# Kernel optimization log

Hardware: AMD Instinct MI355X
Metric: run time of the kernel (lower is better)

Reference implementation:

```python
import jax, jax.numpy as jnp
import numpy as np

N = 50000          # nodes (spots/cells)
E = 1000000        # edges, avg degree 20
IN_DIM, HID, OUT = 256, 128, 64
R = 2              # num_relations
NEG_SLOPE = 0.2    # PyG RGATConv default


def setup_inputs() -> dict:
    key = jax.random.key(0)
    ks = jax.random.split(key, 12)
    features = jax.random.normal(ks[0], (N, IN_DIM), jnp.float32)
    edge_index = jax.random.randint(ks[1], (2, E), 0, N)
    edge_type = jax.random.randint(ks[2], (E,), 0, R)
    s_in, s_hid, s_out = 1.0 / np.sqrt(IN_DIM), 1.0 / np.sqrt(HID), 1.0 / np.sqrt(OUT)
    # RGATConv layer 1 (heads=1, dim=1): relation weights + shared q,k
    W1 = jax.random.normal(ks[3], (R, IN_DIM, HID), jnp.float32) * s_in
    q1 = jax.random.normal(ks[4], (HID, 1), jnp.float32) * s_hid
    k1 = jax.random.normal(ks[5], (HID, 1), jnp.float32) * s_hid
    # RGATConv layer 2
    W2 = jax.random.normal(ks[6], (R, HID, OUT), jnp.float32) * s_hid
    q2 = jax.random.normal(ks[7], (OUT, 1), jnp.float32) * s_out
    k2 = jax.random.normal(ks[8], (OUT, 1), jnp.float32) * s_out
    # decoder: Linear(OUT->HID) then Linear(HID->IN_DIM), biases default-on
    dec_w1 = jax.random.normal(ks[9], (HID, OUT), jnp.float32) * s_out
    dec_b1 = jnp.zeros((HID,), jnp.float32)
    dec_w2 = jax.random.normal(ks[10], (IN_DIM, HID), jnp.float32) * s_hid
    dec_b2 = jnp.zeros((IN_DIM,), jnp.float32)
    return dict(features=features, edge_index=edge_index, edge_type=edge_type,
                W1=W1, q1=q1, k1=k1, W2=W2, q2=q2, k2=k2,
                dec_w1=dec_w1, dec_b1=dec_b1, dec_w2=dec_w2, dec_b2=dec_b2)


def _segment_softmax(alpha, index, num_segments):
    # softmax over edges grouped by destination node (PyG softmax, +1e-16 denom)
    amax = jax.ops.segment_max(alpha, index, num_segments=num_segments)
    amax = jnp.where(jnp.isfinite(amax), amax, 0.0)  # empty segments -> -inf
    ex = jnp.exp(alpha - amax[index])
    denom = jax.ops.segment_sum(ex, index, num_segments=num_segments)
    return ex / (denom[index] + 1e-16)


def _rgat_layer(x, W, q, k, src, dst, edge_type, num_nodes):
    # per-edge x_e @ W[edge_type[e]] == project all nodes per relation, then gather
    proj = jnp.einsum('ni,rio->rno', x, W)          # (R, N, O)
    out_i = proj[edge_type, dst]                    # (E, O) dest-node projection
    out_j = proj[edge_type, src]                    # (E, O) src-node projection
    alpha = jax.nn.leaky_relu(out_i @ q + out_j @ k, NEG_SLOPE)  # (E, 1)
    alpha = _segment_softmax(alpha, dst, num_nodes)
    out = jax.ops.segment_sum(alpha * out_j, dst, num_segments=num_nodes)  # (N, O)
    return out, alpha


def reference(features, edge_index, edge_type, W1, q1, k1, W2, q2, k2,
              dec_w1, dec_b1, dec_w2, dec_b2):
    src, dst = edge_index[0], edge_index[1]
    n = features.shape[0]
    h1, att1 = _rgat_layer(features, W1, q1, k1, src, dst, edge_type, n)
    h1 = jax.nn.elu(h1)
    h2, att2 = _rgat_layer(h1, W2, q2, k2, src, dst, edge_type, n)
    h2 = jax.nn.elu(h2)
    h3 = (h2 @ dec_w1.T + dec_b1) @ dec_w2.T + dec_b2
    return h2, h3, att1, att2
```

## Files before the change

kernel.cpp:

```cpp
#include <hip/hip_runtime.h>
#include <hip/hip_bf16.h>

static constexpr int N_NODES = 50000;
static constexpr int N_EDGE  = 1000000;
static constexpr int IN_D    = 256;
static constexpr int HID_D   = 128;
static constexpr int OUT_D   = 64;
static constexpr int R_REL   = 2;

typedef __attribute__((ext_vector_type(8))) short short8;
typedef __attribute__((ext_vector_type(8))) unsigned short ushort8;
typedef __attribute__((ext_vector_type(4))) float float4v;

static __device__ __forceinline__ unsigned short f2bf(float v) {
    __hip_bfloat16 h = __float2bfloat16(v);
    return *(unsigned short*)&h;
}
static __device__ __forceinline__ float bf2f(unsigned short u) {
    union { unsigned int i; float f; } c; c.i = ((unsigned int)u) << 16; return c.f;
}
static __device__ __forceinline__ float bflo(unsigned u) {
    union { unsigned i; float f; } c; c.i = u << 16; return c.f;
}
static __device__ __forceinline__ float bfhi(unsigned u) {
    union { unsigned i; float f; } c; c.i = u & 0xFFFF0000u; return c.f;
}
static __device__ __forceinline__ float u2f(unsigned u) {
    union { unsigned i; float f; } c; c.i = u; return c.f;
}
static __device__ __forceinline__ unsigned f2u(float f) {
    union { unsigned i; float f; } c; c.f = f; return c.i;
}
static __device__ __forceinline__ void acc8(float w, uint4 v, float (&a)[8]) {
    a[0] = fmaf(w, bflo(v.x), a[0]); a[1] = fmaf(w, bfhi(v.x), a[1]);
    a[2] = fmaf(w, bflo(v.y), a[2]); a[3] = fmaf(w, bfhi(v.y), a[3]);
    a[4] = fmaf(w, bflo(v.z), a[4]); a[5] = fmaf(w, bfhi(v.z), a[5]);
    a[6] = fmaf(w, bflo(v.w), a[6]); a[7] = fmaf(w, bfhi(v.w), a[7]);
}

__global__ __launch_bounds__(256) void prep_k(
    const float* __restrict__ W1, const float* __restrict__ W2,
    const float* __restrict__ dw1, const float* __restrict__ dw2,
    unsigned short* __restrict__ Wc1t, unsigned short* __restrict__ Wc2t,
    unsigned short* __restrict__ dw1h, unsigned short* __restrict__ dw1l,
    unsigned short* __restrict__ dw2h, unsigned short* __restrict__ dw2l)
{
    int idx = blockIdx.x * 256 + threadIdx.x;
    if (idx < R_REL * HID_D * IN_D) {
        const int n = idx / IN_D, kk = idx % IN_D;
        const int r = n / HID_D, o = n % HID_D;
        Wc1t[(long)n * IN_D + kk] = f2bf(W1[((long)r * IN_D + kk) * HID_D + o]);
        return;
    }
    idx -= R_REL * HID_D * IN_D;
    if (idx < R_REL * OUT_D * HID_D) {
        const int n = idx / HID_D, kk = idx % HID_D;
        const int r = n / OUT_D, o = n % OUT_D;
        Wc2t[(long)n * HID_D + kk] = f2bf(W2[((long)r * HID_D + kk) * OUT_D + o]);
        return;
    }
    idx -= R_REL * OUT_D * HID_D;
    if (idx < HID_D * OUT_D) {
        const float v = dw1[idx];
        const unsigned short hi = f2bf(v);
        dw1h[idx] = hi; dw1l[idx] = f2bf(v - bf2f(hi));
        return;
    }
    idx -= HID_D * OUT_D;
    if (idx < IN_D * HID_D) {
        const float v = dw2[idx];
        const unsigned short hi = f2bf(v);
        dw2h[idx] = hi; dw2l[idx] = f2bf(v - bf2f(hi));
    }
}

template<bool CVT>
__global__ __launch_bounds__(256) void gemm_bf16_k(
    const unsigned short* __restrict__ A, const float* __restrict__ Af,
    const unsigned short* __restrict__ Bt,
    unsigned short* __restrict__ Cb, int M, int K, int Nn)
{
    constexpr int BM = 128;
    constexpr int LDK = 40;
    __shared__ __align__(16) unsigned short As[BM * LDK];
    __shared__ __align__(16) unsigned short Bs[128 * LDK];

    const int tid = threadIdx.x;
    const int wave = tid >> 6, lane = tid & 63;
    const int wm = (wave >> 1) * 64;
    const int wn = (wave & 1) * 64;
    const int bm = blockIdx.y * BM;
    const int bn = blockIdx.x * 128;
    const int l15 = lane & 15, quad = lane >> 4;

    const int ar0 = tid >> 2,          ach0 = (tid & 3) * 8;
    const int ar1 = (tid + 256) >> 2,  ach1 = (tid & 3) * 8;
    const long ga0 = (long)min(bm + ar0, M - 1) * K + ach0;
    const long ga1 = (long)min(bm + ar1, M - 1) * K + ach1;
    const long gb0 = (long)(bn + ar0) * K + ach0;
    const long gb1 = (long)(bn + ar1) * K + ach1;

    float4 fa0, fa1, fa2, fa3;
    uint4  qa0, qa1;
    uint4  qb0, qb1;

#define GEMM_PREF(k0) do {                                                  \
    if constexpr (CVT) {                                                    \
        fa0 = *(const float4*)&Af[ga0 + (k0)];                              \
        fa1 = *(const float4*)&Af[ga0 + (k0) + 4];                          \
        fa2 = *(const float4*)&Af[ga1 + (k0)];                              \
        fa3 = *(const float4*)&Af[ga1 + (k0) + 4];                          \
    } else {                                                                \
        qa0 = *(const uint4*)&A[ga0 + (k0)];                                \
        qa1 = *(const uint4*)&A[ga1 + (k0)];                                \
    }                                                                       \
    qb0 = *(const uint4*)&Bt[gb0 + (k0)];                                   \
    qb1 = *(const uint4*)&Bt[gb1 + (k0)];                                   \
} while (0)

#define GEMM_COMMIT() do {                                                  \
    if constexpr (CVT) {                                                    \
        uint4 o0, o1;                                                       \
        o0.x = (unsigned)f2bf(fa0.x) | ((unsigned)f2bf(fa0.y) << 16);       \
        o0.y = (unsigned)f2bf(fa0.z) | ((unsigned)f2bf(fa0.w) << 16);       \
        o0.z = (unsigned)f2bf(fa1.x) | ((unsigned)f2bf(fa1.y) << 16);       \
        o0.w = (unsigned)f2bf(fa1.z) | ((unsigned)f2bf(fa1.w) << 16);       \
        o1.x = (unsigned)f2bf(fa2.x) | ((unsigned)f2bf(fa2.y) << 16);       \
        o1.y = (unsigned)f2bf(fa2.z) | ((unsigned)f2bf(fa2.w) << 16);       \
        o1.z = (unsigned)f2bf(fa3.x) | ((unsigned)f2bf(fa3.y) << 16);       \
        o1.w = (unsigned)f2bf(fa3.z) | ((unsigned)f2bf(fa3.w) << 16);       \
        *(uint4*)&As[ar0 * LDK + ach0] = o0;                                \
        *(uint4*)&As[ar1 * LDK + ach1] = o1;                                \
    } else {                                                                \
        *(uint4*)&As[ar0 * LDK + ach0] = qa0;                               \
        *(uint4*)&As[ar1 * LDK + ach1] = qa1;                               \
    }                                                                       \
    *(uint4*)&Bs[ar0 * LDK + ach0] = qb0;                                   \
    *(uint4*)&Bs[ar1 * LDK + ach1] = qb1;                                   \
} while (0)

    float4v acc[4][4];
#pragma unroll
    for (int i = 0; i < 4; ++i)
#pragma unroll
        for (int j = 0; j < 4; ++j) acc[i][j] = (float4v){0.f, 0.f, 0.f, 0.f};

    GEMM_PREF(0);
    for (int k0 = 0; k0 < K; k0 += 32) {
        GEMM_COMMIT();
        __syncthreads();
        if (k0 + 32 < K) GEMM_PREF(k0 + 32);

        short8 bfrag[4];
#pragma unroll
        for (int nt = 0; nt < 4; ++nt)
            bfrag[nt] = *(const short8*)&Bs[(wn + nt * 16 + l15) * LDK + quad * 8];
#pragma unroll
        for (int mt = 0; mt < 4; ++mt) {
            const short8 afrag = *(const short8*)&As[(wm + mt * 16 + l15) * LDK + quad * 8];
#pragma unroll
            for (int nt = 0; nt < 4; ++nt)
                acc[mt][nt] = __builtin_amdgcn_mfma_f32_16x16x32_bf16(
                    afrag, bfrag[nt], acc[mt][nt], 0, 0, 0);
        }
        __syncthreads();
    }
#undef GEMM_PREF
#undef GEMM_COMMIT

#pragma unroll
    for (int mt = 0; mt < 4; ++mt)
#pragma unroll
        for (int nt = 0; nt < 4; ++nt) {
            const int n = bn + wn + nt * 16 + l15;
#pragma unroll
            for (int rg = 0; rg < 4; ++rg) {
                const int m = bm + wm + mt * 16 + quad * 4 + rg;
                if (m < M) Cb[(long)m * Nn + n] = f2bf(acc[mt][nt][rg]);
            }
        }
}

template<bool SPLITOUT>
__global__ __launch_bounds__(256) void dec_gemm_k(
    const unsigned short* __restrict__ Ah, const unsigned short* __restrict__ Al,
    const unsigned short* __restrict__ Bh, const unsigned short* __restrict__ Bl,
    const float* __restrict__ bias, float* __restrict__ Cf,
    unsigned short* __restrict__ Ch, unsigned short* __restrict__ Cl,
    int M, int K, int Nn)
{
    constexpr int BM = 128;
    constexpr int LDK = 40;
    __shared__ __align__(16) unsigned short Ash[BM * LDK];
    __shared__ __align__(16) unsigned short Asl[BM * LDK];
    __shared__ __align__(16) unsigned short Bsh[128 * LDK];
    __shared__ __align__(16) unsigned short Bsl[128 * LDK];

    const int tid = threadIdx.x;
    const int wave = tid >> 6, lane = tid & 63;
    const int wm = (wave >> 1) * 64;
    const int wn = (wave & 1) * 64;
    const int bm = blockIdx.y * BM;
    const int bn = blockIdx.x * 128;
    const int l15 = lane & 15, quad = lane >> 4;

    const int ar0 = tid >> 2,          ach0 = (tid & 3) * 8;
    const int ar1 = (tid + 256) >> 2,  ach1 = (tid & 3) * 8;
    const long ga0 = (long)min(bm + ar0, M - 1) * K + ach0;
    const long ga1 = (long)min(bm + ar1, M - 1) * K + ach1;
    const long gb0 = (long)(bn + ar0) * K + ach0;
    const long gb1 = (long)(bn + ar1) * K + ach1;

    uint4 ph0, ph1, pl0, pl1;
    uint4 rh0, rh1, rl0, rl1;

#define DEC_PREF(k0) do {                                   \
    ph0 = *(const uint4*)&Ah[ga0 + (k0)];                   \
    ph1 = *(const uint4*)&Ah[ga1 + (k0)];                   \
    pl0 = *(const uint4*)&Al[ga0 + (k0)];                   \
    pl1 = *(const uint4*)&Al[ga1 + (k0)];                   \
    rh0 = *(const uint4*)&Bh[gb0 + (k0)];                   \
    rh1 = *(const uint4*)&Bh[gb1 + (k0)];                   \
    rl0 = *(const uint4*)&Bl[gb0 + (k0)];                   \
    rl1 = *(const uint4*)&Bl[gb1 + (k0)];                   \
} while (0)

#define DEC_COMMIT() do {                                   \
    *(uint4*)&Ash[ar0 * LDK + ach0] = ph0;                  \
    *(uint4*)&Ash[ar1 * LDK + ach1] = ph1;                  \
    *(uint4*)&Asl[ar0 * LDK + ach0] = pl0;                  \
    *(uint4*)&Asl[ar1 * LDK + ach1] = pl1;                  \
    *(uint4*)&Bsh[ar0 * LDK + ach0] = rh0;                  \
    *(uint4*)&Bsh[ar1 * LDK + ach1] = rh1;                  \
    *(uint4*)&Bsl[ar0 * LDK + ach0] = rl0;                  \
    *(uint4*)&Bsl[ar1 * LDK + ach1] = rl1;                  \
} while (0)

    float4v acc[4][4];
#pragma unroll
    for (int i = 0; i < 4; ++i)
#pragma unroll
        for (int j = 0; j < 4; ++j) acc[i][j] = (float4v){0.f, 0.f, 0.f, 0.f};

    DEC_PREF(0);
    for (int k0 = 0; k0 < K; k0 += 32) {
        DEC_COMMIT();
        __syncthreads();
        if (k0 + 32 < K) DEC_PREF(k0 + 32);

        short8 bh[4], bl[4];
#pragma unroll
        for (int nt = 0; nt < 4; ++nt) {
            bh[nt] = *(const short8*)&Bsh[(wn + nt * 16 + l15) * LDK + quad * 8];
            bl[nt] = *(const short8*)&Bsl[(wn + nt * 16 + l15) * LDK + quad * 8];
        }
#pragma unroll
        for (int mt = 0; mt < 4; ++mt) {
            const short8 ah = *(const short8*)&Ash[(wm + mt * 16 + l15) * LDK + quad * 8];
            const short8 al = *(const short8*)&Asl[(wm + mt * 16 + l15) * LDK + quad * 8];
#pragma unroll
            for (int nt = 0; nt < 4; ++nt) {
                acc[mt][nt] = __builtin_amdgcn_mfma_f32_16x16x32_bf16(ah, bh[nt], acc[mt][nt], 0, 0, 0);
                acc[mt][nt] = __builtin_amdgcn_mfma_f32_16x16x32_bf16(al, bh[nt], acc[mt][nt], 0, 0, 0);
                acc[mt][nt] = __builtin_amdgcn_mfma_f32_16x16x32_bf16(ah, bl[nt], acc[mt][nt], 0, 0, 0);
            }
        }
        __syncthreads();
    }
#undef DEC_PREF
#undef DEC_COMMIT

#pragma unroll
    for (int mt = 0; mt < 4; ++mt)
#pragma unroll
        for (int nt = 0; nt < 4; ++nt) {
            const int n = bn + wn + nt * 16 + l15;
            const float bv = bias[n];
#pragma unroll
            for (int rg = 0; rg < 4; ++rg) {
                const int m = bm + wm + mt * 16 + quad * 4 + rg;
                if (m >= M) continue;
                const float v = acc[mt][nt][rg] + bv;
                if (SPLITOUT) {
                    const unsigned short hi = f2bf(v);
                    Ch[(long)m * Nn + n] = hi;
                    Cl[(long)m * Nn + n] = f2bf(v - bf2f(hi));
                } else {
                    Cf[(long)m * Nn + n] = v;
                }
            }
        }
}

template<int D>
__global__ __launch_bounds__(256) void dotsB_k(
    const unsigned short* __restrict__ projb, const float* __restrict__ q,
    const float* __restrict__ k, float* __restrict__ qd, float* __restrict__ kd,
    int Nn)
{
    const int node = (int)((blockIdx.x * (long)blockDim.x + threadIdx.x) >> 6);
    const int lane = threadIdx.x & 63;
    if (node >= Nn) return;
    const unsigned short* row = projb + (long)node * (2 * D);
    float sq0, sk0, sq1, sk1;
    if (D == 128) {
        const ushort2 a = *(const ushort2*)(row + 2 * lane);
        const ushort2 b = *(const ushort2*)(row + 128 + 2 * lane);
        const float q0 = q[2 * lane], q1 = q[2 * lane + 1];
        const float c0 = k[2 * lane], c1 = k[2 * lane + 1];
        const float a0 = bf2f(a.x), a1 = bf2f(a.y);
        const float b0 = bf2f(b.x), b1 = bf2f(b.y);
        sq0 = fmaf(a0, q0, a1 * q1); sk0 = fmaf(a0, c0, a1 * c1);
        sq1 = fmaf(b0, q0, b1 * q1); sk1 = fmaf(b0, c0, b1 * c1);
    } else {
        const float a0 = bf2f(row[lane]), b0 = bf2f(row[64 + lane]);
        const float q0 = q[lane], c0 = k[lane];
        sq0 = a0 * q0; sk0 = a0 * c0;
        sq1 = b0 * q0; sk1 = b0 * c0;
    }
#pragma unroll
    for (int off = 32; off; off >>= 1) {
        sq0 += __shfl_xor(sq0, off); sk0 += __shfl_xor(sk0, off);
        sq1 += __shfl_xor(sq1, off); sk1 += __shfl_xor(sk1, off);
    }
    if (lane == 0) {
        *(float2*)&qd[2 * node] = make_float2(sq0, sq1);
        kd[node] = sk0; kd[Nn + node] = sk1;
    }
}

static constexpr int CPAD = 16;

__global__ __launch_bounds__(256) void rank_k(
    const int* __restrict__ dstv, int* __restrict__ cntp,
    int* __restrict__ rank, int E)
{
    const int e = blockIdx.x * blockDim.x + threadIdx.x;
    if (e >= E) return;
    rank[e] = atomicAdd(&cntp[dstv[e] * CPAD], 1);
}

__global__ __launch_bounds__(256) void scan1_k(
    const int* __restrict__ cntp, int* __restrict__ excl_out,
    int* __restrict__ bsum, int n)
{
    __shared__ int s[256];
    const int t = threadIdx.x;
    const int i = blockIdx.x * 256 + t;
    const int v = (i < n) ? cntp[i * CPAD] : 0;
    s[t] = v;
    __syncthreads();
    for (int off = 1; off < 256; off <<= 1) {
        const int x = (t >= off) ? s[t - off] : 0;
        __syncthreads();
        s[t] += x;
        __syncthreads();
    }
    if (i < n) excl_out[i] = s[t] - v;
    if (t == 255) bsum[blockIdx.x] = s[255];
}

__global__ __launch_bounds__(256) void scan2_k(
    int* __restrict__ bsum, int* __restrict__ bpre, int nb)
{
    __shared__ int s[256];
    const int t = threadIdx.x;
    const int v = (t < nb) ? bsum[t] : 0;
    s[t] = v;
    __syncthreads();
    for (int off = 1; off < 256; off <<= 1) {
        const int x = (t >= off) ? s[t - off] : 0;
        __syncthreads();
        s[t] += x;
        __syncthreads();
    }
    if (t < nb) bpre[t] = s[t] - v;
}

__global__ __launch_bounds__(256) void scan3_k(
    int* __restrict__ excl, const int* __restrict__ bpre,
    int* __restrict__ offs, int n, int total)
{
    const int i = blockIdx.x * 256 + threadIdx.x;
    if (i >= n) return;
    offs[i] = excl[i] + bpre[i >> 8];
    if (i == 0) offs[n] = total;
}

__global__ __launch_bounds__(256) void place_k(
    const int* __restrict__ srcv, const int* __restrict__ dstv,
    const int* __restrict__ et, const int* __restrict__ rank,
    const int* __restrict__ offs, unsigned* __restrict__ recs, int E)
{
    const int e = blockIdx.x * blockDim.x + threadIdx.x;
    if (e >= E) return;
    const int pos = offs[dstv[e]] + rank[e];
    recs[pos] = (unsigned)((et[e] << 16) | srcv[e]);
}

__global__ __launch_bounds__(256) void aggr1_k(
    const int* __restrict__ offs, const unsigned* __restrict__ recs,
    const float* __restrict__ qd, const float* __restrict__ kd,
    const unsigned short* __restrict__ projb,
    float* __restrict__ inv_out, unsigned short* __restrict__ h1b, int Nn)
{
    __shared__ uint2 sh[4][64];
    const int wid = threadIdx.x >> 6;
    const int d = blockIdx.x * 4 + wid;
    const int lane = threadIdx.x & 63;
    if (d >= Nn) return;
    const int beg = offs[d], end = offs[d + 1];
    const float2 qv = *(const float2*)&qd[2 * d];
    const char* pb = (const char*)projb;
    const int quarter = lane >> 4, l15 = lane & 15;
    const unsigned lb = (unsigned)(l15 << 4);
    uint2* shl = sh[wid];

    float exsum = 0.f;
    float a[8] = {0.f, 0.f, 0.f, 0.f, 0.f, 0.f, 0.f, 0.f};

    for (int b = beg; b < end; b += 64) {
        const int i = b + lane;
        float ex = 0.f; unsigned off = 0;
        if (i < end) {
            const unsigned rx = recs[i];
            const int s = (int)(rx & 0xFFFFu), t = (int)(rx >> 16);
            float av = (t ? qv.y : qv.x) + kd[t * Nn + s];
            av = av > 0.f ? av : 0.2f * av;
            ex = __expf(av);
            off = ((unsigned)s << 9) | ((unsigned)t << 8);
        }
        shl[lane] = make_uint2(f2u(ex), off);
        exsum += ex;

        const int cnt = min(64, end - b);
        for (int j = 0; j < cnt; j += 16) {
            const uint2 p0 = shl[j + quarter];
            const uint2 p1 = shl[j + 4 + quarter];
            const uint2 p2 = shl[j + 8 + quarter];
            const uint2 p3 = shl[j + 12 + quarter];
            const uint4 v0 = *(const uint4*)(pb + (p0.y + lb));
            const uint4 v1 = *(const uint4*)(pb + (p1.y + lb));
            const uint4 v2 = *(const uint4*)(pb + (p2.y + lb));
            const uint4 v3 = *(const uint4*)(pb + (p3.y + lb));
            acc8(u2f(p0.x), v0, a);
            acc8(u2f(p1.x), v1, a);
            acc8(u2f(p2.x), v2, a);
            acc8(u2f(p3.x), v3, a);
        }
    }
#pragma unroll
    for (int o = 32; o; o >>= 1) exsum += __shfl_xor(exsum, o);
    const float inv = 1.f / (exsum + 1e-16f);
    if (lane == 0) inv_out[d] = inv;
#pragma unroll
    for (int q = 0; q < 8; ++q) {
        a[q] += __shfl_xor(a[q], 32);
        a[q] += __shfl_xor(a[q], 16);
    }
    if (quarter == 0) {
        ushort8 st;
#pragma unroll
        for (int q = 0; q < 8; ++q) {
            const float e = a[q] * inv;
            st[q] = f2bf(e > 0.f ? e : expm1f(e));
        }
        *(ushort8*)&h1b[(long)d * 128 + (l15 << 3)] = st;
    }
}

__global__ __launch_bounds__(256) void aggr2_k(
    const int* __restrict__ offs, const unsigned* __restrict__ recs,
    const float* __restrict__ qd, const float* __restrict__ kd,
    const unsigned short* __restrict__ projb,
    float* __restrict__ inv_out, float* __restrict__ out,
    unsigned short* __restrict__ h2h, unsigned short* __restrict__ h2l, int Nn)
{
    __shared__ uint2 sh[4][64];
    const int wid = threadIdx.x >> 6;
    const int d = blockIdx.x * 4 + wid;
    const int lane = threadIdx.x & 63;
    if (d >= Nn) return;
    const int beg = offs[d], end = offs[d + 1];
    const float2 qv = *(const float2*)&qd[2 * d];
    const char* pb = (const char*)projb;
    const int eighth = lane >> 3, l7 = lane & 7;
    const unsigned lb = (unsigned)(l7 << 4);
    uint2* shl = sh[wid];

    float exsum = 0.f;
    float a[8] = {0.f, 0.f, 0.f, 0.f, 0.f, 0.f, 0.f, 0.f};

    for (int b = beg; b < end; b += 64) {
        const int i = b + lane;
        float ex = 0.f; unsigned off = 0;
        if (i < end) {
            const unsigned rx = recs[i];
            const int s = (int)(rx & 0xFFFFu), t = (int)(rx >> 16);
            float av = (t ? qv.y : qv.x) + kd[t * Nn + s];
            av = av > 0.f ? av : 0.2f * av;
            ex = __expf(av);
            off = ((unsigned)s << 8) | ((unsigned)t << 7);
        }
        shl[lane] = make_uint2(f2u(ex), off);
        exsum += ex;

        const int cnt = min(64, end - b);
        for (int j = 0; j < cnt; j += 32) {
            const uint2 p0 = shl[j + eighth];
            const uint2 p1 = shl[j + 8 + eighth];
            const uint2 p2 = shl[j + 16 + eighth];
            const uint2 p3 = shl[j + 24 + eighth];
            const uint4 v0 = *(const uint4*)(pb + (p0.y + lb));
            const uint4 v1 = *(const uint4*)(pb + (p1.y + lb));
            const uint4 v2 = *(const uint4*)(pb + (p2.y + lb));
            const uint4 v3 = *(const uint4*)(pb + (p3.y + lb));
            acc8(u2f(p0.x), v0, a);
            acc8(u2f(p1.x), v1, a);
            acc8(u2f(p2.x), v2, a);
            acc8(u2f(p3.x), v3, a);
        }
    }
#pragma unroll
    for (int o = 32; o; o >>= 1) exsum += __shfl_xor(exsum, o);
    const float inv = 1.f / (exsum + 1e-16f);
    if (lane == 0) inv_out[d] = inv;
#pragma unroll
    for (int q = 0; q < 8; ++q) {
        a[q] += __shfl_xor(a[q], 32);
        a[q] += __shfl_xor(a[q], 16);
        a[q] += __shfl_xor(a[q], 8);
    }
    if (eighth == 0) {
        float vv[8];
#pragma unroll
        for (int q = 0; q < 8; ++q) {
            const float e = a[q] * inv;
            vv[q] = e > 0.f ? e : expm1f(e);
        }
        float4 f0; f0.x = vv[0]; f0.y = vv[1]; f0.z = vv[2]; f0.w = vv[3];
        float4 f1; f1.x = vv[4]; f1.y = vv[5]; f1.z = vv[6]; f1.w = vv[7];
        *(float4*)&out[(long)d * 64 + (l7 << 3)] = f0;
        *(float4*)&out[(long)d * 64 + (l7 << 3) + 4] = f1;
        ushort8 hh, hl;
#pragma unroll
        for (int q = 0; q < 8; ++q) {
            const unsigned short hi = f2bf(vv[q]);
            hh[q] = hi; hl[q] = f2bf(vv[q] - bf2f(hi));
        }
        *(ushort8*)&h2h[(long)d * 64 + (l7 << 3)] = hh;
        *(ushort8*)&h2l[(long)d * 64 + (l7 << 3)] = hl;
    }
}

__global__ __launch_bounds__(256) void att_k(
    const int* __restrict__ srcv, const int* __restrict__ dstv,
    const int* __restrict__ et,
    const float* __restrict__ qd1, const float* __restrict__ kd1,
    const float* __restrict__ inv1,
    const float* __restrict__ qd2, const float* __restrict__ kd2,
    const float* __restrict__ inv2,
    float* __restrict__ att1, float* __restrict__ att2, int E, int Nn)
{
    const int e = blockIdx.x * 256 + threadIdx.x;
    if (e >= E) return;
    const int s = srcv[e], d = dstv[e], t = et[e];
    float x1 = qd1[2 * d + t] + kd1[t * Nn + s];
    x1 = x1 > 0.f ? x1 : 0.2f * x1;
    att1[e] = __expf(x1) * inv1[d];
    float x2 = qd2[2 * d + t] + kd2[t * Nn + s];
    x2 = x2 > 0.f ? x2 : 0.2f * x2;
    att2[e] = __expf(x2) * inv2[d];
}

extern "C" void kernel_launch(void* const* d_in, const int* in_sizes, int n_in,
                              void* d_out, int out_size, void* d_ws, size_t ws_size,
                              hipStream_t stream)
{
    const float* features = (const float*)d_in[0];
    const int*   eidx     = (const int*)d_in[1];
    const int*   etype    = (const int*)d_in[2];
    const float* W1       = (const float*)d_in[3];
    const float* q1       = (const float*)d_in[4];
    const float* k1       = (const float*)d_in[5];
    const float* W2       = (const float*)d_in[6];
    const float* q2       = (const float*)d_in[7];
    const float* k2       = (const float*)d_in[8];
    const float* dw1      = (const float*)d_in[9];
    const float* db1      = (const float*)d_in[10];
    const float* dw2      = (const float*)d_in[11];
    const float* db2      = (const float*)d_in[12];

    const int* srcv = eidx;
    const int* dstv = eidx + N_EDGE;

    float* out_h2 = (float*)d_out;
    float* out_h3 = out_h2 + (long)N_NODES * OUT_D;
    float* att1   = out_h3 + (long)N_NODES * IN_D;
    float* att2   = att1 + N_EDGE;

    char* W = (char*)d_ws;
    int* rank = (int*)W;
    unsigned short* projb1 = (unsigned short*)(W);
    unsigned short* projb2 = (unsigned short*)(W);
    unsigned short* hidh   = (unsigned short*)(W);
    unsigned short* hidl   = (unsigned short*)(W + 12800000);
    unsigned short* h1b    = (unsigned short*)(W + 25600000);
    unsigned short* h2h    = (unsigned short*)(W + 25600000 + 12800000);
    unsigned short* h2l    = (unsigned short*)(W + 25600000 + 19200000);
    float* qd1 = (float*)(W + 51200000);
    float* kd1 = qd1 + 2 * N_NODES;
    float* qd2 = kd1 + 2 * N_NODES;
    float* kd2 = qd2 + 2 * N_NODES;
    int* offs   = (int*)(kd2 + 2 * N_NODES);
    int* bsum   = offs + N_NODES + 1;
    int* bpre   = bsum + 256;
    int* excl   = bpre + 256;
    float* inv1 = (float*)(W + 53500000);
    float* inv2 = inv1 + N_NODES;
    int* cntp   = (int*)(W + 53900000);
    unsigned* recs = (unsigned*)(W + 57300000);
    unsigned short* Wc1t = (unsigned short*)(W + 65300000);
    unsigned short* Wc2t = Wc1t + 65536;
    unsigned short* dw1h = Wc2t + 16384;
    unsigned short* dw1l = dw1h + 8192;
    unsigned short* dw2h = dw1l + 8192;
    unsigned short* dw2l = dw2h + 32768;

    const int NB = (N_NODES + 255) / 256;
    const int MB128 = (N_NODES + 127) / 128;

    prep_k<<<480, 256, 0, stream>>>(W1, W2, dw1, dw2,
                                    Wc1t, Wc2t, dw1h, dw1l, dw2h, dw2l);

    hipMemsetAsync(cntp, 0, sizeof(int) * N_NODES * CPAD, stream);
    rank_k<<<(N_EDGE + 255) / 256, 256, 0, stream>>>(dstv, cntp, rank, N_EDGE);
    scan1_k<<<NB, 256, 0, stream>>>(cntp, excl, bsum, N_NODES);
    scan2_k<<<1, 256, 0, stream>>>(bsum, bpre, NB);
    scan3_k<<<NB, 256, 0, stream>>>(excl, bpre, offs, N_NODES, N_EDGE);
    place_k<<<(N_EDGE + 255) / 256, 256, 0, stream>>>(
        srcv, dstv, etype, rank, offs, recs, N_EDGE);

    gemm_bf16_k<true><<<dim3(2, MB128), 256, 0, stream>>>(
        nullptr, features, Wc1t, projb1, N_NODES, IN_D, 2 * HID_D);
    dotsB_k<128><<<(int)(((long)N_NODES * 64 + 255) / 256), 256, 0, stream>>>(
        projb1, q1, k1, qd1, kd1, N_NODES);
    aggr1_k<<<(N_NODES + 3) / 4, 256, 0, stream>>>(
        offs, recs, qd1, kd1, projb1, inv1, h1b, N_NODES);

    gemm_bf16_k<false><<<dim3(1, MB128), 256, 0, stream>>>(
        h1b, nullptr, Wc2t, projb2, N_NODES, HID_D, 2 * OUT_D);
    dotsB_k<64><<<(int)(((long)N_NODES * 64 + 255) / 256), 256, 0, stream>>>(
        projb2, q2, k2, qd2, kd2, N_NODES);
    aggr2_k<<<(N_NODES + 3) / 4, 256, 0, stream>>>(
        offs, recs, qd2, kd2, projb2, inv2, out_h2, h2h, h2l, N_NODES);

    att_k<<<(N_EDGE + 255) / 256, 256, 0, stream>>>(
        srcv, dstv, etype, qd1, kd1, inv1, qd2, kd2, inv2, att1, att2,
        N_EDGE, N_NODES);

    dec_gemm_k<true><<<dim3(1, MB128), 256, 0, stream>>>(
        h2h, h2l, dw1h, dw1l, db1, nullptr, hidh, hidl, N_NODES, OUT_D, HID_D);
    dec_gemm_k<false><<<dim3(2, MB128), 256, 0, stream>>>(
        hidh, hidl, dw2h, dw2l, db2, out_h3, nullptr, nullptr, N_NODES, HID_D, IN_D);
}
```

Baseline: 396.7 us.

## Fuse attention dot products into GEMM epilogue and merge scan kernels

Computes the per-node q and k attention dot products inside the projection GEMM epilogue, using wave shuffles and atomicAdd into pre-zeroed buffers. This removes the two separate dotsB kernels that re-read the projected rows. The two scan-finishing kernels are merged into one, with every block redoing the tiny block-sum scan. The memset is replaced by zeroing inside prep_k, which also covers the q/k accumulators. Atomics make the float summation order nondeterministic, and the epilogue uses the fp32 accumulators rather than bf16-rounded values.

```diff
diff --git a/kernel.cpp b/kernel.cpp
--- a/kernel.cpp
+++ b/kernel.cpp
@@ -43,7 +43,8 @@
     const float* __restrict__ dw1, const float* __restrict__ dw2,
     unsigned short* __restrict__ Wc1t, unsigned short* __restrict__ Wc2t,
     unsigned short* __restrict__ dw1h, unsigned short* __restrict__ dw1l,
-    unsigned short* __restrict__ dw2h, unsigned short* __restrict__ dw2l)
+    unsigned short* __restrict__ dw2h, unsigned short* __restrict__ dw2l,
+    uint4* __restrict__ zeroA, uint4* __restrict__ zeroB)
 {
     int idx = blockIdx.x * 256 + threadIdx.x;
     if (idx < R_REL * HID_D * IN_D) {
@@ -71,6 +72,16 @@
         const float v = dw2[idx];
         const unsigned short hi = f2bf(v);
         dw2h[idx] = hi; dw2l[idx] = f2bf(v - bf2f(hi));
+        return;
+    }
+    idx -= IN_D * HID_D;
+    if (idx < 100000) {
+        zeroA[idx] = make_uint4(0, 0, 0, 0);
+        return;
+    }
+    idx -= 100000;
+    if (idx < 200000) {
+        zeroB[idx] = make_uint4(0, 0, 0, 0);
     }
 }
 
@@ -78,7 +89,10 @@
 __global__ __launch_bounds__(256) void gemm_bf16_k(
     const unsigned short* __restrict__ A, const float* __restrict__ Af,
     const unsigned short* __restrict__ Bt,
-    unsigned short* __restrict__ Cb, int M, int K, int Nn)
+    unsigned short* __restrict__ Cb,
+    const float* __restrict__ qvec, const float* __restrict__ kvec,
+    float* __restrict__ qdo, float* __restrict__ kdo, int Dq,
+    int M, int K, int Nn)
 {
     constexpr int BM = 128;
     constexpr int LDK = 40;
@@ -179,6 +193,34 @@
                 if (m < M) Cb[(long)m * Nn + n] = f2bf(acc[mt][nt][rg]);
             }
         }
+
+    {
+        const int r = (bn + wn) / Dq;
+        const int obase = bn + wn - r * Dq + l15;
+#pragma unroll
+        for (int mt = 0; mt < 4; ++mt)
+#pragma unroll
+            for (int rg = 0; rg < 4; ++rg) {
+                float qp = 0.f, kp = 0.f;
+#pragma unroll
+                for (int nt = 0; nt < 4; ++nt) {
+                    const float cv = acc[mt][nt][rg];
+                    qp = fmaf(cv, qvec[obase + nt * 16], qp);
+                    kp = fmaf(cv, kvec[obase + nt * 16], kp);
+                }
+                qp += __shfl_xor(qp, 1); kp += __shfl_xor(kp, 1);
+                qp += __shfl_xor(qp, 2); kp += __shfl_xor(kp, 2);
+                qp += __shfl_xor(qp, 4); kp += __shfl_xor(kp, 4);
+                qp += __shfl_xor(qp, 8); kp += __shfl_xor(kp, 8);
+                if (l15 == 0) {
+                    const int m = bm + wm + mt * 16 + quad * 4 + rg;
+                    if (m < M) {
+                        atomicAdd(&qdo[2 * m + r], qp);
+                        atomicAdd(&kdo[(long)r * M + m], kp);
+                    }
+                }
+            }
+    }
 }
 
 template<bool SPLITOUT>
@@ -292,43 +334,6 @@
         }
 }
 
-template<int D>
-__global__ __launch_bounds__(256) void dotsB_k(
-    const unsigned short* __restrict__ projb, const float* __restrict__ q,
-    const float* __restrict__ k, float* __restrict__ qd, float* __restrict__ kd,
-    int Nn)
-{
-    const int node = (int)((blockIdx.x * (long)blockDim.x + threadIdx.x) >> 6);
-    const int lane = threadIdx.x & 63;
-    if (node >= Nn) return;
-    const unsigned short* row = projb + (long)node * (2 * D);
-    float sq0, sk0, sq1, sk1;
-    if (D == 128) {
-        const ushort2 a = *(const ushort2*)(row + 2 * lane);
-        const ushort2 b = *(const ushort2*)(row + 128 + 2 * lane);
-        const float q0 = q[2 * lane], q1 = q[2 * lane + 1];
-        const float c0 = k[2 * lane], c1 = k[2 * lane + 1];
-        const float a0 = bf2f(a.x), a1 = bf2f(a.y);
-        const float b0 = bf2f(b.x), b1 = bf2f(b.y);
-        sq0 = fmaf(a0, q0, a1 * q1); sk0 = fmaf(a0, c0, a1 * c1);
-        sq1 = fmaf(b0, q0, b1 * q1); sk1 = fmaf(b0, c0, b1 * c1);
-    } else {
-        const float a0 = bf2f(row[lane]), b0 = bf2f(row[64 + lane]);
-        const float q0 = q[lane], c0 = k[lane];
-        sq0 = a0 * q0; sk0 = a0 * c0;
-        sq1 = b0 * q0; sk1 = b0 * c0;
-    }
-#pragma unroll
-    for (int off = 32; off; off >>= 1) {
-        sq0 += __shfl_xor(sq0, off); sk0 += __shfl_xor(sk0, off);
-        sq1 += __shfl_xor(sq1, off); sk1 += __shfl_xor(sk1, off);
-    }
-    if (lane == 0) {
-        *(float2*)&qd[2 * node] = make_float2(sq0, sq1);
-        kd[node] = sk0; kd[Nn + node] = sk1;
-    }
-}
-
 static constexpr int CPAD = 16;
 
 __global__ __launch_bounds__(256) void rank_k(
@@ -360,10 +365,12 @@
     if (t == 255) bsum[blockIdx.x] = s[255];
 }
 
-__global__ __launch_bounds__(256) void scan2_k(
-    int* __restrict__ bsum, int* __restrict__ bpre, int nb)
+__global__ __launch_bounds__(256) void scan23_k(
+    const int* __restrict__ excl, const int* __restrict__ bsum,
+    int* __restrict__ offs, int n, int total, int nb)
 {
     __shared__ int s[256];
+    __shared__ int base;
     const int t = threadIdx.x;
     const int v = (t < nb) ? bsum[t] : 0;
     s[t] = v;
@@ -374,16 +381,10 @@
         s[t] += x;
         __syncthreads();
     }
-    if (t < nb) bpre[t] = s[t] - v;
-}
-
-__global__ __launch_bounds__(256) void scan3_k(
-    int* __restrict__ excl, const int* __restrict__ bpre,
-    int* __restrict__ offs, int n, int total)
-{
-    const int i = blockIdx.x * 256 + threadIdx.x;
-    if (i >= n) return;
-    offs[i] = excl[i] + bpre[i >> 8];
+    if (t == (int)blockIdx.x) base = s[t] - v;
+    __syncthreads();
+    const int i = blockIdx.x * 256 + t;
+    if (i < n) offs[i] = excl[i] + base;
     if (i == 0) offs[n] = total;
 }
 
@@ -630,28 +631,25 @@
     const int NB = (N_NODES + 255) / 256;
     const int MB128 = (N_NODES + 127) / 128;
 
-    prep_k<<<480, 256, 0, stream>>>(W1, W2, dw1, dw2,
-                                    Wc1t, Wc2t, dw1h, dw1l, dw2h, dw2l);
-
-    hipMemsetAsync(cntp, 0, sizeof(int) * N_NODES * CPAD, stream);
+    prep_k<<<1652, 256, 0, stream>>>(W1, W2, dw1, dw2,
+                                     Wc1t, Wc2t, dw1h, dw1l, dw2h, dw2l,
+                                     (uint4*)qd1, (uint4*)cntp);
+
     rank_k<<<(N_EDGE + 255) / 256, 256, 0, stream>>>(dstv, cntp, rank, N_EDGE);
     scan1_k<<<NB, 256, 0, stream>>>(cntp, excl, bsum, N_NODES);
-    scan2_k<<<1, 256, 0, stream>>>(bsum, bpre, NB);
-    scan3_k<<<NB, 256, 0, stream>>>(excl, bpre, offs, N_NODES, N_EDGE);
+    scan23_k<<<NB, 256, 0, stream>>>(excl, bsum, offs, N_NODES, N_EDGE, NB);
     place_k<<<(N_EDGE + 255) / 256, 256, 0, stream>>>(
         srcv, dstv, etype, rank, offs, recs, N_EDGE);
 
     gemm_bf16_k<true><<<dim3(2, MB128), 256, 0, stream>>>(
-        nullptr, features, Wc1t, projb1, N_NODES, IN_D, 2 * HID_D);
-    dotsB_k<128><<<(int)(((long)N_NODES * 64 + 255) / 256), 256, 0, stream>>>(
-        projb1, q1, k1, qd1, kd1, N_NODES);
+        nullptr, features, Wc1t, projb1, q1, k1, qd1, kd1, HID_D,
+        N_NODES, IN_D, 2 * HID_D);
     aggr1_k<<<(N_NODES + 3) / 4, 256, 0, stream>>>(
         offs, recs, qd1, kd1, projb1, inv1, h1b, N_NODES);
 
     gemm_bf16_k<false><<<dim3(1, MB128), 256, 0, stream>>>(
-        h1b, nullptr, Wc2t, projb2, N_NODES, HID_D, 2 * OUT_D);
-    dotsB_k<64><<<(int)(((long)N_NODES * 64 + 255) / 256), 256, 0, stream>>>(
-        projb2, q2, k2, qd2, kd2, N_NODES);
+        h1b, nullptr, Wc2t, projb2, q2, k2, qd2, kd2, OUT_D,
+        N_NODES, HID_D, 2 * OUT_D);
     aggr2_k<<<(N_NODES + 3) / 4, 256, 0, stream>>>(
         offs, recs, qd2, kd2, projb2, inv2, out_h2, h2h, h2l, N_NODES);
 
```

Measured after the change: 385.1 us. 1.03x faster.
